# Optimization experiments

Hardware: AMD Instinct MI355X
Metric: run time of the kernel (lower is better)

Reference implementation:

```python
import jax, jax.numpy as jnp
import numpy as np

N_DRUG = 846
D = 256          # embedding_num
K = 128          # neighbor_sample_size
N_REL = 200
N_ENT = 100000
BN_EPS = 1e-5


def setup_inputs() -> dict:
    key = jax.random.key(0)
    ks = jax.random.split(key, 12)
    drug_name = jnp.arange(N_DRUG, dtype=jnp.int64) if jax.config.jax_enable_x64 else jnp.arange(N_DRUG, dtype=jnp.int32)
    adj_tail = jax.random.randint(ks[0], (N_DRUG, K), 0, N_ENT)
    adj_relation = jax.random.randint(ks[1], (N_DRUG, K), 0, N_REL)
    drug_table = jax.random.normal(ks[2], (N_DRUG, D), dtype=jnp.float32)
    rela_table = jax.random.normal(ks[3], (N_REL, D), dtype=jnp.float32)
    ent_table = jax.random.normal(ks[4], (N_ENT, D), dtype=jnp.float32)
    W1 = jax.random.normal(ks[5], (N_DRUG, D, D), dtype=jnp.float32) * 0.05
    b1 = jax.random.normal(ks[6], (K, D), dtype=jnp.float32) * 0.05
    W2 = jax.random.normal(ks[7], (N_DRUG, D, D), dtype=jnp.float32) * 0.05
    b2 = jax.random.normal(ks[8], (K, D), dtype=jnp.float32) * 0.05
    # Linear(2D -> D), xavier-uniform weight, zero bias
    lim = np.sqrt(6.0 / (2 * D + D)).astype(np.float32)
    lin_w = jax.random.uniform(ks[9], (D, 2 * D), minval=-lim, maxval=lim, dtype=jnp.float32)
    lin_b = jnp.zeros((D,), dtype=jnp.float32)
    bn_gamma = jnp.ones((D,), dtype=jnp.float32)
    bn_beta = jnp.zeros((D,), dtype=jnp.float32)
    return {
        "drug_name": drug_name, "adj_tail": adj_tail, "adj_relation": adj_relation,
        "drug_table": drug_table, "rela_table": rela_table, "ent_table": ent_table,
        "W1": W1, "b1": b1, "W2": W2, "b2": b2,
        "lin_w": lin_w, "lin_b": lin_b, "bn_gamma": bn_gamma, "bn_beta": bn_beta,
    }


def reference(drug_name, adj_tail, adj_relation, drug_table, rela_table, ent_table,
              W1, b1, W2, b2, lin_w, lin_b, bn_gamma, bn_beta):
    drug_emb = drug_table[drug_name]                  # [N, D]
    rela_emb = rela_table[adj_relation]               # [N, K, D]
    ent_emb = ent_table[adj_tail]                     # [N, K, D]

    drug_rel = drug_emb[:, None, :] * rela_emb        # [N, K, D]
    h = jnp.einsum('nkd,nde->nke', drug_rel, W1) + b1 # per-drug bmm + bias
    h = jax.nn.relu(h)
    h = jnp.einsum('nkd,nde->nke', h, W2) + b2        # [N, K, D]

    score = jnp.sum(h, axis=-1, keepdims=True)        # [N, K, 1]
    score = jax.nn.softmax(score, axis=1)             # softmax over neighbors

    weighted_ent = jnp.einsum('nk,nkd->nd', score[..., 0], ent_emb)  # [N, D]
    drug_e = jnp.concatenate([weighted_ent, drug_emb], axis=1)       # [N, 2D]

    x = drug_e @ lin_w.T + lin_b                      # Linear(2D -> D)
    x = jax.nn.relu(x)
    # BatchNorm1d in training mode: biased batch statistics
    mean = jnp.mean(x, axis=0)
    var = jnp.var(x, axis=0)
    drug_f = bn_gamma * (x - mean) * jax.lax.rsqrt(var + BN_EPS) + bn_beta
    return drug_f
```

## Files before the change

kernel.cpp:

```cpp
#include <hip/hip_runtime.h>
#include <math.h>

#define NDRUG 846
#define DIM   256
#define KN    128

typedef _Float16 half8 __attribute__((ext_vector_type(8)));
typedef float f32x4 __attribute__((ext_vector_type(4)));

__global__ __launch_bounds__(256) void b2sum_kernel(const float* __restrict__ b2,
                                                    float* __restrict__ b2sum) {
    int row  = blockIdx.x * 4 + (threadIdx.x >> 6);
    int lane = threadIdx.x & 63;
    if (row >= KN) return;
    float4 v = *((const float4*)(b2 + (size_t)row * DIM) + lane);
    float s = v.x + v.y + v.z + v.w;
    #pragma unroll
    for (int off = 32; off >= 1; off >>= 1) s += __shfl_xor(s, off);
    if (lane == 0) b2sum[row] = s;
}

__global__ __launch_bounds__(256, 3) void gnn_main(
    const int* __restrict__ adj_tail, const int* __restrict__ adj_rel,
    const float* __restrict__ drug_table, const float* __restrict__ rela_table,
    const float* __restrict__ ent_table,
    const float* __restrict__ W1, const float* __restrict__ b1,
    const float* __restrict__ W2, const float* __restrict__ b2sum,
    float* __restrict__ drug_e)
{
    __shared__ __align__(16) float s_drug[DIM];
    __shared__ __align__(16) float s_w2[DIM];
    __shared__ int   s_ridx[KN];
    __shared__ int   s_tidx[KN];
    __shared__ float s_score[KN];
    __shared__ float s_scoreP[4][KN];
    __shared__ float s_red[8];
    __shared__ __align__(16) half8 sB[2][8][64];
    __shared__ __align__(16) _Float16 sA[2][4][520];

    const int n    = blockIdx.x;
    const int t    = threadIdx.x;
    const int wv   = t >> 6;
    const int lane = t & 63;

    s_drug[t] = drug_table[(size_t)n * DIM + t];
    s_w2[t]   = 0.f;
    if (t < KN) {
        s_ridx[t]  = adj_rel[(size_t)n * KN + t];
        s_tidx[t]  = adj_tail[(size_t)n * KN + t];
        s_score[t] = b2sum[t];
    }
    __syncthreads();

    const int kk = t >> 1;
    const int o0 = (t & 1) << 1;
    const float* rrow = rela_table + (size_t)s_ridx[kk] * DIM;
    const int dd = t >> 3;
    const int e0 = (t & 7) << 3;
    const int qj_q = dd >> 3, qj_j = dd & 7;
    const float* W1n = W1 + (size_t)n * DIM * DIM;
    const float* W2n = W2 + (size_t)n * DIM * DIM;

    float sacc[8] = {0.f,0.f,0.f,0.f,0.f,0.f,0.f,0.f};

    auto stageA = [&](int s, int buf) {
        const int d0 = s << 5;
        #pragma unroll
        for (int i = 0; i < 2; ++i) {
            const int o  = o0 | i;
            const int db = d0 + (o << 3);
            float4 p0 = *(const float4*)(rrow + db);
            float4 p1 = *(const float4*)(rrow + db + 4);
            float4 q0 = *(const float4*)(s_drug + db);
            float4 q1 = *(const float4*)(s_drug + db + 4);
            half8 h;
            h[0] = (_Float16)(p0.x * q0.x);
            h[1] = (_Float16)(p0.y * q0.y);
            h[2] = (_Float16)(p0.z * q0.z);
            h[3] = (_Float16)(p0.w * q0.w);
            h[4] = (_Float16)(p1.x * q1.x);
            h[5] = (_Float16)(p1.y * q1.y);
            h[6] = (_Float16)(p1.z * q1.z);
            h[7] = (_Float16)(p1.w * q1.w);
            sB[buf][kk >> 4][(kk & 15) | (o << 4)] = h;
        }
    };
    auto stageW = [&](int c, int s, int buf) {
        const int d0 = s << 5;
        const float* src = W1n + (size_t)(d0 + dd) * DIM + (c << 6) + e0;
        float4 p0 = *(const float4*)src;
        float4 p1 = *(const float4*)(src + 4);
        float f[8] = {p0.x, p0.y, p0.z, p0.w, p1.x, p1.y, p1.z, p1.w};
        #pragma unroll
        for (int u = 0; u < 8; ++u) {
            const int el = e0 + u;
            sA[buf][el >> 4][(((el & 15) | (qj_q << 4)) << 3) + qj_j] = (_Float16)f[u];
        }
    };
    auto w2step = [&](int s) {
        const int d0 = s << 5;
        const float* wr = W2n + (size_t)(d0 + dd) * DIM + ((t & 7) << 2);
        float sum = 0.f;
        #pragma unroll
        for (int u = 0; u < 8; ++u) {
            float4 v = *(const float4*)(wr + (u << 5));
            sum += (v.x + v.y) + (v.z + v.w);
        }
        sum += __shfl_xor(sum, 1);
        sum += __shfl_xor(sum, 2);
        sum += __shfl_xor(sum, 4);
        if ((t & 7) == 0) s_w2[d0 + dd] = sum;
    };

    const int kcol = lane & 15, quad = lane >> 4;

    for (int c = 0; c < 4; ++c) {
        f32x4 acc[8] = {};
        stageA(0, 0);
        stageW(c, 0, 0);
        for (int s = 0; s < 8; ++s) {
            __syncthreads();
            if (c == 0) w2step(s);
            if (s < 7) { stageA(s + 1, (s + 1) & 1); stageW(c, s + 1, (s + 1) & 1); }
            const int buf = s & 1;
            half8 af = *(const half8*)&sA[buf][wv][(size_t)lane << 3];
            #pragma unroll
            for (int kt = 0; kt < 8; ++kt) {
                half8 bf = sB[buf][kt][lane];
                acc[kt] = __builtin_amdgcn_mfma_f32_16x16x32_f16(af, bf, acc[kt], 0, 0, 0);
            }
        }
        if (c == 0) __syncthreads();
        const int ebase = (c << 6) + (wv << 4) + (quad << 2);
        float4 ww = *(const float4*)(s_w2 + ebase);
        #pragma unroll
        for (int kt = 0; kt < 8; ++kt) {
            const int k = (kt << 4) + kcol;
            float4 bb = *(const float4*)(b1 + (size_t)k * DIM + ebase);
            f32x4 a = acc[kt];
            sacc[kt] += fmaxf(a[0] + bb.x, 0.f) * ww.x
                      + fmaxf(a[1] + bb.y, 0.f) * ww.y
                      + fmaxf(a[2] + bb.z, 0.f) * ww.z
                      + fmaxf(a[3] + bb.w, 0.f) * ww.w;
        }
    }

    #pragma unroll
    for (int kt = 0; kt < 8; ++kt) {
        float v = sacc[kt];
        v += __shfl_xor(v, 16);
        v += __shfl_xor(v, 32);
        if (lane < 16) s_scoreP[wv][(kt << 4) + lane] = v;
    }
    __syncthreads();
    if (t < KN)
        s_score[t] += (s_scoreP[0][t] + s_scoreP[1][t]) + (s_scoreP[2][t] + s_scoreP[3][t]);
    __syncthreads();

    float sc = (t < KN) ? s_score[t] : -3.0e38f;
    float mx = sc;
    #pragma unroll
    for (int off = 32; off >= 1; off >>= 1) mx = fmaxf(mx, __shfl_xor(mx, off));
    if (lane == 0) s_red[wv] = mx;
    __syncthreads();
    float M = fmaxf(fmaxf(s_red[0], s_red[1]), fmaxf(s_red[2], s_red[3]));
    float ex = (t < KN) ? expf(sc - M) : 0.f;
    float ssum = ex;
    #pragma unroll
    for (int off = 32; off >= 1; off >>= 1) ssum += __shfl_xor(ssum, off);
    if (lane == 0) s_red[4 + wv] = ssum;
    __syncthreads();
    float S = (s_red[4] + s_red[5]) + (s_red[6] + s_red[7]);
    if (t < KN) s_score[t] = ex / S;
    __syncthreads();

    float a0 = 0.f, a1 = 0.f, a2 = 0.f, a3 = 0.f;
    for (int k = 0; k < KN; k += 4) {
        a0 += s_score[k + 0] * ent_table[(size_t)s_tidx[k + 0] * DIM + t];
        a1 += s_score[k + 1] * ent_table[(size_t)s_tidx[k + 1] * DIM + t];
        a2 += s_score[k + 2] * ent_table[(size_t)s_tidx[k + 2] * DIM + t];
        a3 += s_score[k + 3] * ent_table[(size_t)s_tidx[k + 3] * DIM + t];
    }
    drug_e[(size_t)n * 512 + t]       = (a0 + a1) + (a2 + a3);
    drug_e[(size_t)n * 512 + DIM + t] = s_drug[t];
}

__global__ __launch_bounds__(256) void linear_kernel(
    const float* __restrict__ drug_e, const float* __restrict__ lin_w,
    const float* __restrict__ lin_b,
    float* __restrict__ x, float* __restrict__ g_sum, float* __restrict__ g_sumsq)
{
    __shared__ __align__(16) float s_de[4][512];
    const int b = blockIdx.x, t = threadIdx.x;
    const int n0 = b * 4;
    #pragma unroll
    for (int ss = 0; ss < 2; ++ss) {
        int idx = ss * 256 + t;
        int row = idx >> 7, col4 = idx & 127;
        float4 v = make_float4(0.f, 0.f, 0.f, 0.f);
        if (n0 + row < NDRUG) v = *((const float4*)(drug_e + (size_t)(n0 + row) * 512) + col4);
        *(float4*)&s_de[row][col4 * 4] = v;
    }
    __syncthreads();
    float acc[4] = {};
    const float4* wrow = (const float4*)(lin_w + (size_t)t * 512);
    #pragma unroll 4
    for (int d4 = 0; d4 < 128; ++d4) {
        float4 w = wrow[d4];
        #pragma unroll
        for (int i = 0; i < 4; ++i) {
            float4 de = *(const float4*)&s_de[i][d4 * 4];
            acc[i] += w.x * de.x + w.y * de.y + w.z * de.z + w.w * de.w;
        }
    }
    float bias = lin_b[t];
    float psum = 0.f, psq = 0.f;
    #pragma unroll
    for (int i = 0; i < 4; ++i) {
        if (n0 + i < NDRUG) {
            float v = fmaxf(acc[i] + bias, 0.f);
            x[(size_t)(n0 + i) * DIM + t] = v;
            psum += v; psq += v * v;
        }
    }
    atomicAdd(&g_sum[t], psum);
    atomicAdd(&g_sumsq[t], psq);
}

__global__ __launch_bounds__(256) void bn_kernel(
    const float* __restrict__ x, const float* __restrict__ g_sum,
    const float* __restrict__ g_sumsq,
    const float* __restrict__ gamma, const float* __restrict__ beta,
    float* __restrict__ out)
{
    const int n = blockIdx.x, e = threadIdx.x;
    const float inv = 1.0f / (float)NDRUG;
    float mean = g_sum[e] * inv;
    float var  = fmaxf(g_sumsq[e] * inv - mean * mean, 0.f);
    float rstd = rsqrtf(var + 1e-5f);
    float v = x[(size_t)n * DIM + e];
    out[(size_t)n * DIM + e] = gamma[e] * (v - mean) * rstd + beta[e];
}

extern "C" void kernel_launch(void* const* d_in, const int* in_sizes, int n_in,
                              void* d_out, int out_size, void* d_ws, size_t ws_size,
                              hipStream_t stream) {
    const int*   adj_tail   = (const int*)d_in[1];
    const int*   adj_rel    = (const int*)d_in[2];
    const float* drug_table = (const float*)d_in[3];
    const float* rela_table = (const float*)d_in[4];
    const float* ent_table  = (const float*)d_in[5];
    const float* W1         = (const float*)d_in[6];
    const float* b1         = (const float*)d_in[7];
    const float* W2         = (const float*)d_in[8];
    const float* b2         = (const float*)d_in[9];
    const float* lin_w      = (const float*)d_in[10];
    const float* lin_b      = (const float*)d_in[11];
    const float* gamma      = (const float*)d_in[12];
    const float* beta       = (const float*)d_in[13];
    float* out = (float*)d_out;

    float* ws      = (float*)d_ws;
    float* b2sum   = ws;
    float* drug_e  = ws + 128;
    float* xbuf    = drug_e + (size_t)NDRUG * 512;
    float* g_sum   = xbuf + (size_t)NDRUG * DIM;
    float* g_sumsq = g_sum + DIM;

    hipMemsetAsync(g_sum, 0, 2 * DIM * sizeof(float), stream);
    b2sum_kernel<<<KN / 4, 256, 0, stream>>>(b2, b2sum);
    gnn_main<<<NDRUG, 256, 0, stream>>>(adj_tail, adj_rel, drug_table, rela_table,
                                        ent_table, W1, b1, W2, b2sum, drug_e);
    linear_kernel<<<(NDRUG + 3) / 4, 256, 0, stream>>>(drug_e, lin_w, lin_b,
                                                       xbuf, g_sum, g_sumsq);
    bn_kernel<<<NDRUG, 256, 0, stream>>>(xbuf, g_sum, g_sumsq, gamma, beta, out);
}
```

Before: 606.0 us.

## Split W2 row-sum and entity gather into separate kernels, register-prefetch W1

Moves the W2 row-sum reduction out of gnn_main into its own grid-stride kernel and moves the softmax-weighted entity gather into a separate gather kernel, with scores passed through workspace. Inside gnn_main, all eight drug·relation B tiles are staged to shared memory once, and W1 is prefetched into registers two steps ahead across a single 32-step loop. A raw lgkmcnt wait plus barrier replaces __syncthreads. Occupancy is lowered to 2 blocks per CU to fit the larger shared-memory footprint. The goal is to overlap HBM streaming of W1 with MFMA work and to shorten the critical path of the main kernel. The cost is two extra launches and extra global round-trips for the W2 sums and the scores.

```diff
diff --git a/kernel.cpp b/kernel.cpp
--- a/kernel.cpp
+++ b/kernel.cpp
@@ -20,130 +20,127 @@
     if (lane == 0) b2sum[row] = s;
 }
 
-__global__ __launch_bounds__(256, 3) void gnn_main(
-    const int* __restrict__ adj_tail, const int* __restrict__ adj_rel,
+__global__ __launch_bounds__(256) void w2sum_kernel(const float* __restrict__ W2,
+                                                    float* __restrict__ w2s) {
+    const int nrows = NDRUG * DIM;
+    const int nw    = (gridDim.x * 256) >> 6;
+    const int wid   = (blockIdx.x * 256 + threadIdx.x) >> 6;
+    const int lane  = threadIdx.x & 63;
+    for (int r = wid; r < nrows; r += nw) {
+        float4 v = *((const float4*)(W2 + (size_t)r * DIM) + lane);
+        float s = (v.x + v.y) + (v.z + v.w);
+        #pragma unroll
+        for (int off = 32; off >= 1; off >>= 1) s += __shfl_xor(s, off);
+        if (lane == 0) w2s[r] = s;
+    }
+}
+
+__global__ __launch_bounds__(256, 2) void gnn_main(
+    const int* __restrict__ adj_rel,
     const float* __restrict__ drug_table, const float* __restrict__ rela_table,
-    const float* __restrict__ ent_table,
     const float* __restrict__ W1, const float* __restrict__ b1,
-    const float* __restrict__ W2, const float* __restrict__ b2sum,
-    float* __restrict__ drug_e)
-{
+    const float* __restrict__ b2sum, const float* __restrict__ w2s,
+    float* __restrict__ score_out)
+{
+    __shared__ __align__(16) half8 sB[8][8][64];
+    __shared__ __align__(16) _Float16 sA[2][4][520];
     __shared__ __align__(16) float s_drug[DIM];
-    __shared__ __align__(16) float s_w2[DIM];
+    __shared__ float s_w2[DIM];
     __shared__ int   s_ridx[KN];
-    __shared__ int   s_tidx[KN];
-    __shared__ float s_score[KN];
     __shared__ float s_scoreP[4][KN];
     __shared__ float s_red[8];
-    __shared__ __align__(16) half8 sB[2][8][64];
-    __shared__ __align__(16) _Float16 sA[2][4][520];
 
     const int n    = blockIdx.x;
     const int t    = threadIdx.x;
     const int wv   = t >> 6;
     const int lane = t & 63;
 
+    const float* W1n   = W1 + (size_t)n * DIM * DIM;
+    const float* wbase = W1n + (size_t)(wv << 3) * DIM + lane;
+    float PA[8], PB[8];
+    {
+        #pragma unroll
+        for (int j = 0; j < 8; ++j) PA[j] = wbase[(size_t)j * DIM];
+        const float* p1 = wbase + (size_t)32 * DIM;
+        #pragma unroll
+        for (int j = 0; j < 8; ++j) PB[j] = p1[(size_t)j * DIM];
+    }
+
     s_drug[t] = drug_table[(size_t)n * DIM + t];
-    s_w2[t]   = 0.f;
-    if (t < KN) {
-        s_ridx[t]  = adj_rel[(size_t)n * KN + t];
-        s_tidx[t]  = adj_tail[(size_t)n * KN + t];
-        s_score[t] = b2sum[t];
-    }
-    __syncthreads();
-
-    const int kk = t >> 1;
-    const int o0 = (t & 1) << 1;
-    const float* rrow = rela_table + (size_t)s_ridx[kk] * DIM;
-    const int dd = t >> 3;
-    const int e0 = (t & 7) << 3;
-    const int qj_q = dd >> 3, qj_j = dd & 7;
-    const float* W1n = W1 + (size_t)n * DIM * DIM;
-    const float* W2n = W2 + (size_t)n * DIM * DIM;
-
+    s_w2[t]   = w2s[(size_t)n * DIM + t];
+    float sc_init = 0.f;
+    if (t < KN) { s_ridx[t] = adj_rel[(size_t)n * KN + t]; sc_init = b2sum[t]; }
+    __syncthreads();
+
+    {
+        const int kk = t >> 1, o0 = (t & 1) << 1;
+        const float* rrow = rela_table + (size_t)s_ridx[kk] * DIM;
+        #pragma unroll 2
+        for (int s8 = 0; s8 < 8; ++s8) {
+            #pragma unroll
+            for (int i = 0; i < 2; ++i) {
+                const int o  = o0 | i;
+                const int db = (s8 << 5) + (o << 3);
+                float4 p0 = *(const float4*)(rrow + db);
+                float4 p1 = *(const float4*)(rrow + db + 4);
+                float4 q0 = *(const float4*)(s_drug + db);
+                float4 q1 = *(const float4*)(s_drug + db + 4);
+                half8 h;
+                h[0] = (_Float16)(p0.x * q0.x);
+                h[1] = (_Float16)(p0.y * q0.y);
+                h[2] = (_Float16)(p0.z * q0.z);
+                h[3] = (_Float16)(p0.w * q0.w);
+                h[4] = (_Float16)(p1.x * q1.x);
+                h[5] = (_Float16)(p1.y * q1.y);
+                h[6] = (_Float16)(p1.z * q1.z);
+                h[7] = (_Float16)(p1.w * q1.w);
+                sB[s8][kk >> 4][(kk & 15) | (o << 4)] = h;
+            }
+        }
+    }
+
+    const int kcol = lane & 15, quad = lane >> 4;
+    f32x4 acc[8] = {};
     float sacc[8] = {0.f,0.f,0.f,0.f,0.f,0.f,0.f,0.f};
-
-    auto stageA = [&](int s, int buf) {
-        const int d0 = s << 5;
-        #pragma unroll
-        for (int i = 0; i < 2; ++i) {
-            const int o  = o0 | i;
-            const int db = d0 + (o << 3);
-            float4 p0 = *(const float4*)(rrow + db);
-            float4 p1 = *(const float4*)(rrow + db + 4);
-            float4 q0 = *(const float4*)(s_drug + db);
-            float4 q1 = *(const float4*)(s_drug + db + 4);
-            half8 h;
-            h[0] = (_Float16)(p0.x * q0.x);
-            h[1] = (_Float16)(p0.y * q0.y);
-            h[2] = (_Float16)(p0.z * q0.z);
-            h[3] = (_Float16)(p0.w * q0.w);
-            h[4] = (_Float16)(p1.x * q1.x);
-            h[5] = (_Float16)(p1.y * q1.y);
-            h[6] = (_Float16)(p1.z * q1.z);
-            h[7] = (_Float16)(p1.w * q1.w);
-            sB[buf][kk >> 4][(kk & 15) | (o << 4)] = h;
-        }
-    };
-    auto stageW = [&](int c, int s, int buf) {
-        const int d0 = s << 5;
-        const float* src = W1n + (size_t)(d0 + dd) * DIM + (c << 6) + e0;
-        float4 p0 = *(const float4*)src;
-        float4 p1 = *(const float4*)(src + 4);
-        float f[8] = {p0.x, p0.y, p0.z, p0.w, p1.x, p1.y, p1.z, p1.w};
-        #pragma unroll
-        for (int u = 0; u < 8; ++u) {
-            const int el = e0 + u;
-            sA[buf][el >> 4][(((el & 15) | (qj_q << 4)) << 3) + qj_j] = (_Float16)f[u];
-        }
-    };
-    auto w2step = [&](int s) {
-        const int d0 = s << 5;
-        const float* wr = W2n + (size_t)(d0 + dd) * DIM + ((t & 7) << 2);
-        float sum = 0.f;
-        #pragma unroll
-        for (int u = 0; u < 8; ++u) {
-            float4 v = *(const float4*)(wr + (u << 5));
-            sum += (v.x + v.y) + (v.z + v.w);
-        }
-        sum += __shfl_xor(sum, 1);
-        sum += __shfl_xor(sum, 2);
-        sum += __shfl_xor(sum, 4);
-        if ((t & 7) == 0) s_w2[d0 + dd] = sum;
-    };
-
-    const int kcol = lane & 15, quad = lane >> 4;
-
-    for (int c = 0; c < 4; ++c) {
-        f32x4 acc[8] = {};
-        stageA(0, 0);
-        stageW(c, 0, 0);
-        for (int s = 0; s < 8; ++s) {
-            __syncthreads();
-            if (c == 0) w2step(s);
-            if (s < 7) { stageA(s + 1, (s + 1) & 1); stageW(c, s + 1, (s + 1) & 1); }
-            const int buf = s & 1;
-            half8 af = *(const half8*)&sA[buf][wv][(size_t)lane << 3];
+    const f32x4 fzero = {};
+
+    auto step = [&](int ss, float (&P)[8]) {
+        half8 hw;
+        #pragma unroll
+        for (int j = 0; j < 8; ++j) hw[j] = (_Float16)P[j];
+        *(half8*)&sA[ss & 1][lane >> 4][((lane & 15) | (wv << 4)) << 3] = hw;
+        if (ss + 2 < 32) {
+            const float* p = wbase + (size_t)(((ss + 2) & 7) << 5) * DIM
+                                   + (((ss + 2) >> 3) << 6);
+            #pragma unroll
+            for (int j = 0; j < 8; ++j) P[j] = p[(size_t)j * DIM];
+        }
+        asm volatile("s_waitcnt lgkmcnt(0)\n\ts_barrier" ::: "memory");
+        half8 af = *(const half8*)&sA[ss & 1][wv][(size_t)lane << 3];
+        const int ds = ss & 7;
+        #pragma unroll
+        for (int kt = 0; kt < 8; ++kt) {
+            half8 bf = sB[ds][kt][lane];
+            acc[kt] = __builtin_amdgcn_mfma_f32_16x16x32_f16(af, bf, acc[kt], 0, 0, 0);
+        }
+        if (ds == 7) {
+            const int c = ss >> 3;
+            const int ebase = (c << 6) + (wv << 4) + (quad << 2);
+            float4 ww = *(const float4*)(s_w2 + ebase);
             #pragma unroll
             for (int kt = 0; kt < 8; ++kt) {
-                half8 bf = sB[buf][kt][lane];
-                acc[kt] = __builtin_amdgcn_mfma_f32_16x16x32_f16(af, bf, acc[kt], 0, 0, 0);
+                const int k = (kt << 4) + kcol;
+                float4 bb = *(const float4*)(b1 + (size_t)k * DIM + ebase);
+                f32x4 a = acc[kt];
+                sacc[kt] += fmaxf(a[0] + bb.x, 0.f) * ww.x
+                          + fmaxf(a[1] + bb.y, 0.f) * ww.y
+                          + fmaxf(a[2] + bb.z, 0.f) * ww.z
+                          + fmaxf(a[3] + bb.w, 0.f) * ww.w;
+                acc[kt] = fzero;
             }
         }
-        if (c == 0) __syncthreads();
-        const int ebase = (c << 6) + (wv << 4) + (quad << 2);
-        float4 ww = *(const float4*)(s_w2 + ebase);
-        #pragma unroll
-        for (int kt = 0; kt < 8; ++kt) {
-            const int k = (kt << 4) + kcol;
-            float4 bb = *(const float4*)(b1 + (size_t)k * DIM + ebase);
-            f32x4 a = acc[kt];
-            sacc[kt] += fmaxf(a[0] + bb.x, 0.f) * ww.x
-                      + fmaxf(a[1] + bb.y, 0.f) * ww.y
-                      + fmaxf(a[2] + bb.z, 0.f) * ww.z
-                      + fmaxf(a[3] + bb.w, 0.f) * ww.w;
-        }
-    }
+    };
+    for (int sp = 0; sp < 16; ++sp) { step(2 * sp, PA); step(2 * sp + 1, PB); }
 
     #pragma unroll
     for (int kt = 0; kt < 8; ++kt) {
@@ -153,11 +150,10 @@
         if (lane < 16) s_scoreP[wv][(kt << 4) + lane] = v;
     }
     __syncthreads();
+    float sc = -3.0e38f;
     if (t < KN)
-        s_score[t] += (s_scoreP[0][t] + s_scoreP[1][t]) + (s_scoreP[2][t] + s_scoreP[3][t]);
-    __syncthreads();
-
-    float sc = (t < KN) ? s_score[t] : -3.0e38f;
+        sc = sc_init + (s_scoreP[0][t] + s_scoreP[1][t]) + (s_scoreP[2][t] + s_scoreP[3][t]);
+
     float mx = sc;
     #pragma unroll
     for (int off = 32; off >= 1; off >>= 1) mx = fmaxf(mx, __shfl_xor(mx, off));
@@ -171,18 +167,39 @@
     if (lane == 0) s_red[4 + wv] = ssum;
     __syncthreads();
     float S = (s_red[4] + s_red[5]) + (s_red[6] + s_red[7]);
-    if (t < KN) s_score[t] = ex / S;
-    __syncthreads();
-
-    float a0 = 0.f, a1 = 0.f, a2 = 0.f, a3 = 0.f;
-    for (int k = 0; k < KN; k += 4) {
-        a0 += s_score[k + 0] * ent_table[(size_t)s_tidx[k + 0] * DIM + t];
-        a1 += s_score[k + 1] * ent_table[(size_t)s_tidx[k + 1] * DIM + t];
-        a2 += s_score[k + 2] * ent_table[(size_t)s_tidx[k + 2] * DIM + t];
-        a3 += s_score[k + 3] * ent_table[(size_t)s_tidx[k + 3] * DIM + t];
-    }
-    drug_e[(size_t)n * 512 + t]       = (a0 + a1) + (a2 + a3);
-    drug_e[(size_t)n * 512 + DIM + t] = s_drug[t];
+    if (t < KN) score_out[(size_t)n * KN + t] = ex / S;
+}
+
+__global__ __launch_bounds__(256) void gather_kernel(
+    const float* __restrict__ score, const int* __restrict__ adj_tail,
+    const float* __restrict__ ent_table, const float* __restrict__ drug_table,
+    float* __restrict__ drug_e)
+{
+    __shared__ float s_p[KN];
+    __shared__ int   s_ti[KN];
+    const int n = blockIdx.x, t = threadIdx.x;
+    if (t < KN) {
+        s_p[t]  = score[(size_t)n * KN + t];
+        s_ti[t] = adj_tail[(size_t)n * KN + t];
+    }
+    __syncthreads();
+    float a0=0.f,a1=0.f,a2=0.f,a3=0.f,a4=0.f,a5=0.f,a6=0.f,a7=0.f;
+    for (int k = 0; k < KN; k += 8) {
+        float v0 = ent_table[(size_t)s_ti[k + 0] * DIM + t];
+        float v1 = ent_table[(size_t)s_ti[k + 1] * DIM + t];
+        float v2 = ent_table[(size_t)s_ti[k + 2] * DIM + t];
+        float v3 = ent_table[(size_t)s_ti[k + 3] * DIM + t];
+        float v4 = ent_table[(size_t)s_ti[k + 4] * DIM + t];
+        float v5 = ent_table[(size_t)s_ti[k + 5] * DIM + t];
+        float v6 = ent_table[(size_t)s_ti[k + 6] * DIM + t];
+        float v7 = ent_table[(size_t)s_ti[k + 7] * DIM + t];
+        a0 += s_p[k + 0] * v0;  a1 += s_p[k + 1] * v1;
+        a2 += s_p[k + 2] * v2;  a3 += s_p[k + 3] * v3;
+        a4 += s_p[k + 4] * v4;  a5 += s_p[k + 5] * v5;
+        a6 += s_p[k + 6] * v6;  a7 += s_p[k + 7] * v7;
+    }
+    drug_e[(size_t)n * 512 + t]       = ((a0 + a1) + (a2 + a3)) + ((a4 + a5) + (a6 + a7));
+    drug_e[(size_t)n * 512 + DIM + t] = drug_table[(size_t)n * DIM + t];
 }
 
 __global__ __launch_bounds__(256) void linear_kernel(
@@ -263,14 +280,19 @@
     float* ws      = (float*)d_ws;
     float* b2sum   = ws;
     float* drug_e  = ws + 128;
+    float* w2s     = drug_e;
     float* xbuf    = drug_e + (size_t)NDRUG * 512;
+    float* score_w = xbuf;
     float* g_sum   = xbuf + (size_t)NDRUG * DIM;
     float* g_sumsq = g_sum + DIM;
 
     hipMemsetAsync(g_sum, 0, 2 * DIM * sizeof(float), stream);
     b2sum_kernel<<<KN / 4, 256, 0, stream>>>(b2, b2sum);
-    gnn_main<<<NDRUG, 256, 0, stream>>>(adj_tail, adj_rel, drug_table, rela_table,
-                                        ent_table, W1, b1, W2, b2sum, drug_e);
+    w2sum_kernel<<<2048, 256, 0, stream>>>(W2, w2s);
+    gnn_main<<<NDRUG, 256, 0, stream>>>(adj_rel, drug_table, rela_table,
+                                        W1, b1, b2sum, w2s, score_w);
+    gather_kernel<<<NDRUG, 256, 0, stream>>>(score_w, adj_tail, ent_table,
+                                             drug_table, drug_e);
     linear_kernel<<<(NDRUG + 3) / 4, 256, 0, stream>>>(drug_e, lin_w, lin_b,
                                                        xbuf, g_sum, g_sumsq);
     bn_kernel<<<NDRUG, 256, 0, stream>>>(xbuf, g_sum, g_sumsq, gamma, beta, out);
```

After: 555.9 us. -8.3%, faster.
